# Performance work log

Measured on AMD Instinct MI355X. Metric: run time of the kernel, lower is better.

## Reference

```python
import jax, jax.numpy as jnp
import numpy as np

LATENT = 2000
N_GROUPS = 10000  # loci_count // window_size
KERNEL = 20       # window_size * 2; per-group input length is 1 so out length == KERNEL
BATCH = 128
EPS = 1e-5
SLOPE = 0.1


def setup_inputs() -> dict:
    key = jax.random.key(0)
    k1, k2, k3, k4, k5 = jax.random.split(key, 5)
    return {
        "z": jax.random.normal(k1, (BATCH, LATENT), dtype=jnp.float32),
        "W_fc": jax.random.normal(k2, (N_GROUPS, LATENT), dtype=jnp.float32) * 0.02,
        "b_fc": jax.random.normal(k3, (N_GROUPS,), dtype=jnp.float32) * 0.02,
        "gamma": jnp.ones((N_GROUPS,), dtype=jnp.float32),
        "beta": jnp.zeros((N_GROUPS,), dtype=jnp.float32),
        "conv_w": jax.random.normal(k4, (N_GROUPS, KERNEL), dtype=jnp.float32) * 0.1,
        "conv_b": jax.random.normal(k5, (N_GROUPS,), dtype=jnp.float32) * 0.02,
    }


def reference(z, W_fc, b_fc, gamma, beta, conv_w, conv_b):
    # Linear: (B, L) @ (L, G) -> (B, G)
    h = jnp.einsum("bl,gl->bg", z, W_fc) + b_fc
    # BatchNorm1d (training mode: biased batch statistics, eps=1e-5)
    mean = jnp.mean(h, axis=0)
    var = jnp.mean(jnp.square(h - mean), axis=0)
    h = (h - mean) * jax.lax.rsqrt(var + EPS) * gamma + beta
    h = jnp.where(h >= 0, h, SLOPE * h)  # LeakyReLU(0.1)
    # Grouped ConvTranspose1d with per-group input length 1 degenerates to
    # an outer product per channel: y[b,g,k] = h[b,g]*w[g,k] + b[g]
    y = h[:, :, None] * conv_w[None, :, :] + conv_b[None, :, None]  # (B, G, K)
    y = jnp.where(y >= 0, y, SLOPE * y)  # LeakyReLU(0.1)
    out = jax.nn.sigmoid(y.reshape(z.shape[0], N_GROUPS * KERNEL))
    return out
```

## Files before the change

### kernel.cpp

```cpp
#include <hip/hip_runtime.h>
#include <hip/hip_bf16.h>
#include <stdint.h>

#define BATCH 128
#define LAT   2000
#define NG    10000
#define KW    20
#define OUTW  (NG * KW)
#define EPSV  1e-5f

#define BK    64
#define NKT   32

#define EG        16
#define HR_STRIDE 132

typedef __bf16 bf16x8 __attribute__((ext_vector_type(8)));
typedef float  f32x4  __attribute__((ext_vector_type(4)));

__device__ __forceinline__ ushort f2bf(float f) {
  uint32_t u = __builtin_bit_cast(uint32_t, f);
  u = (u + 0x7FFFu + ((u >> 16) & 1u)) >> 16;
  return (ushort)u;
}

__device__ __forceinline__ int4 pack8(const float* p) {
  float4 f0 = *(const float4*)p;
  float4 f1 = *(const float4*)(p + 4);
  int4 v;
  v.x = (int)((uint32_t)f2bf(f0.x) | ((uint32_t)f2bf(f0.y) << 16));
  v.y = (int)((uint32_t)f2bf(f0.z) | ((uint32_t)f2bf(f0.w) << 16));
  v.z = (int)((uint32_t)f2bf(f1.x) | ((uint32_t)f2bf(f1.y) << 16));
  v.w = (int)((uint32_t)f2bf(f1.z) | ((uint32_t)f2bf(f1.w) << 16));
  return v;
}

__device__ __forceinline__ void gload_lds16(const void* g, void* l) {
  __builtin_amdgcn_global_load_lds(
      (const __attribute__((address_space(1))) unsigned int*)g,
      (__attribute__((address_space(3))) unsigned int*)l, 16, 0, 0);
}

__global__ __launch_bounds__(256) void zprep_kernel(
    const float* __restrict__ zp, int4* __restrict__ zswz) {
  const int cg = blockIdx.x * 256 + threadIdx.x;
  const int kt = cg >> 10;
  const int c  = cg & 1023;
  const int r  = c >> 3, j = c & 7;
  const int sc = j ^ (r & 7);
  const int k0 = kt * 64 + sc * 8;
  int4 v = make_int4(0, 0, 0, 0);
  if (k0 < LAT) v = pack8(zp + (size_t)r * LAT + k0);
  zswz[cg] = v;
}

__global__ __launch_bounds__(256, 4) void fused16_kernel(
    const int4* __restrict__ zswz, const float* __restrict__ wp,
    const float* __restrict__ gammap, const float* __restrict__ betap,
    const float* __restrict__ convwp, const float* __restrict__ convbp,
    float* __restrict__ out) {
  const int tid = threadIdx.x;
  const int g0  = blockIdx.x * EG;

  __shared__ __attribute__((aligned(16))) ushort Zs[BATCH * BK];
  __shared__ __attribute__((aligned(16))) ushort Ws[EG * BK];
  __shared__ float  h_raw[EG * HR_STRIDE];
  __shared__ float4 cw_s[EG * 5];
  __shared__ float  cb_s[EG];
  __shared__ float  scale_s[EG];
  __shared__ float  shift_s[EG];

  if (tid < EG * 5)
    cw_s[tid] = *(const float4*)(convwp + (size_t)g0 * KW + tid * 4);
  if (tid < EG) cb_s[tid] = convbp[g0 + tid];

  const int lane = tid & 63;
  const int w    = tid >> 6;
  const int q    = lane >> 4;
  const int cl   = lane & 15;

  f32x4 acc[2];
  const f32x4 vzero = {0.f, 0.f, 0.f, 0.f};
  acc[0] = vzero; acc[1] = vzero;

  for (int it = 0; it < NKT; ++it) {
    __syncthreads();

    const int4* zt = zswz + (size_t)it * 1024;
#pragma unroll
    for (int i = 0; i < 4; ++i) {
      int c = i * 256 + tid;
      gload_lds16(zt + c, &Zs[c * 8]);
    }
    if (tid < 128) {
      int r = tid >> 3, j = tid & 7;
      int gk = it * BK + j * 8;
      int4 v = make_int4(0, 0, 0, 0);
      if (gk < LAT) v = pack8(wp + (size_t)(g0 + r) * LAT + gk);
      *(int4*)&Ws[r * BK + ((j ^ (r & 7)) << 3)] = v;
    }
    __syncthreads();

#pragma unroll
    for (int kk = 0; kk < 2; ++kk) {
      int sc = kk * 4 + q;
      bf16x8 af = *(const bf16x8*)&Ws[cl * BK + ((sc ^ (cl & 7)) << 3)];
#pragma unroll
      for (int nt = 0; nt < 2; ++nt) {
        int rb = w * 32 + nt * 16 + cl;
        bf16x8 bfr = *(const bf16x8*)&Zs[rb * BK + ((sc ^ (rb & 7)) << 3)];
        acc[nt] = __builtin_amdgcn_mfma_f32_16x16x32_bf16(af, bfr, acc[nt],
                                                          0, 0, 0);
      }
    }
  }

#pragma unroll
  for (int nt = 0; nt < 2; ++nt)
#pragma unroll
    for (int r = 0; r < 4; ++r)
      h_raw[(q * 4 + r) * HR_STRIDE + w * 32 + nt * 16 + cl] = acc[nt][r];
  __syncthreads();

  float sm[2], sq[2];
#pragma unroll
  for (int half = 0; half < 2; ++half) {
    const int idx = tid + half * 256;
    const int gl  = idx >> 5;
    const int bb  = (idx & 31) * 4;
    const float4 a = *(const float4*)&h_raw[gl * HR_STRIDE + bb];
    sm[half] = a.x + a.y + a.z + a.w;
    sq[half] = a.x * a.x + a.y * a.y + a.z * a.z + a.w * a.w;
  }
#pragma unroll
  for (int m = 1; m < 32; m <<= 1) {
    sm[0] += __shfl_xor(sm[0], m); sq[0] += __shfl_xor(sq[0], m);
    sm[1] += __shfl_xor(sm[1], m); sq[1] += __shfl_xor(sq[1], m);
  }
  if ((tid & 31) == 0) {
#pragma unroll
    for (int half = 0; half < 2; ++half) {
      const int gl = (tid >> 5) + half * 8;
      float mean = sm[half] * (1.f / 128.f);
      float var  = sq[half] * (1.f / 128.f) - mean * mean;
      var = (var < 0.f) ? 0.f : var;
      float inv   = __builtin_amdgcn_rsqf(var + EPSV);
      float scale = inv * gammap[g0 + gl];
      scale_s[gl] = scale;
      shift_s[gl] = betap[g0 + gl] - mean * scale;
    }
  }
  __syncthreads();

  if (tid < 240) {
    const int col4 = tid % 80;
    const int r0   = tid / 80;
    const int gl   = col4 / 5;
    const float4 w4  = cw_s[col4];
    const float  cb  = cb_s[gl];
    const float  scl = scale_s[gl];
    const float  sft = shift_s[gl];
    const float* hsrc = &h_raw[gl * HR_STRIDE];
    float* obase = out + (size_t)g0 * KW + (size_t)col4 * 4;
    for (int j = 0; j < 43; ++j) {
      const int row = j * 3 + r0;
      if (row < BATCH) {
        float h = hsrc[row];
        h = fmaf(h, scl, sft);
        h = fmaxf(h, h * 0.1f);
        float y0 = fmaf(h, w4.x, cb);
        float y1 = fmaf(h, w4.y, cb);
        float y2 = fmaf(h, w4.z, cb);
        float y3 = fmaf(h, w4.w, cb);
        y0 = fmaxf(y0, y0 * 0.1f);
        y1 = fmaxf(y1, y1 * 0.1f);
        y2 = fmaxf(y2, y2 * 0.1f);
        y3 = fmaxf(y3, y3 * 0.1f);
        float4 ov;
        ov.x = __builtin_amdgcn_rcpf(1.f + exp2f(y0 * -1.44269504f));
        ov.y = __builtin_amdgcn_rcpf(1.f + exp2f(y1 * -1.44269504f));
        ov.z = __builtin_amdgcn_rcpf(1.f + exp2f(y2 * -1.44269504f));
        ov.w = __builtin_amdgcn_rcpf(1.f + exp2f(y3 * -1.44269504f));
        *(float4*)(obase + (size_t)row * OUTW) = ov;
      }
    }
  }
}

__global__ __launch_bounds__(256, 2) void fused_decoder_kernel(
    const float* __restrict__ zp, const float* __restrict__ wp,
    const float* __restrict__ gammap, const float* __restrict__ betap,
    const float* __restrict__ convwp, const float* __restrict__ convbp,
    float* __restrict__ out) {
  const int tid = threadIdx.x;
  const int g0  = blockIdx.x * 32;

  __shared__ ushort As[BATCH * BK];
  __shared__ ushort Bs[32 * BK];
  __shared__ float statS[2][2][16];
  __shared__ float statQ[2][2][16];

  const int lane = tid & 63;
  const int w    = tid >> 6;
  const int wm   = w & 1;
  const int wn   = w >> 1;
  const int q    = lane >> 4;
  const int cl   = lane & 15;

  f32x4 acc[4];
  const f32x4 vzero = {0.f, 0.f, 0.f, 0.f};
#pragma unroll
  for (int i = 0; i < 4; ++i) acc[i] = vzero;

  for (int it = 0; it < 32; ++it) {
    const int k0 = it * BK;
    __syncthreads();
#pragma unroll
    for (int i = 0; i < 4; ++i) {
      int c = i * 256 + tid;
      int r = c >> 3, sc = c & 7;
      int gk = k0 + sc * 8;
      int4 v = make_int4(0, 0, 0, 0);
      if (gk < LAT) v = pack8(zp + (size_t)r * LAT + gk);
      *(int4*)&As[r * BK + ((sc ^ (r & 7)) << 3)] = v;
    }
    {
      int r = tid >> 3, sc = tid & 7;
      int g  = g0 + r;
      int gk = k0 + sc * 8;
      int4 v = make_int4(0, 0, 0, 0);
      if (gk < LAT && g < NG) v = pack8(wp + (size_t)g * LAT + gk);
      *(int4*)&Bs[r * BK + ((sc ^ (r & 7)) << 3)] = v;
    }
    __syncthreads();
#pragma unroll
    for (int kk = 0; kk < 2; ++kk) {
      int sc = kk * 4 + q;
      bf16x8 af[4], bfr;
#pragma unroll
      for (int mt = 0; mt < 4; ++mt) {
        int ra = wm * 64 + mt * 16 + cl;
        af[mt] = *(const bf16x8*)&As[ra * BK + ((sc ^ (ra & 7)) << 3)];
      }
      {
        int rb = wn * 16 + cl;
        bfr = *(const bf16x8*)&Bs[rb * BK + ((sc ^ (rb & 7)) << 3)];
      }
#pragma unroll
      for (int mt = 0; mt < 4; ++mt)
        acc[mt] = __builtin_amdgcn_mfma_f32_16x16x32_bf16(af[mt], bfr,
                                                          acc[mt], 0, 0, 0);
    }
  }

  float s = 0.f, ss = 0.f;
#pragma unroll
  for (int mt = 0; mt < 4; ++mt)
#pragma unroll
    for (int r = 0; r < 4; ++r) {
      float v = acc[mt][r];
      s += v; ss += v * v;
    }
  s += __shfl_xor(s, 16); ss += __shfl_xor(ss, 16);
  s += __shfl_xor(s, 32); ss += __shfl_xor(ss, 32);
  if (q == 0) { statS[wm][wn][cl] = s; statQ[wm][wn][cl] = ss; }
  __syncthreads();

  const int gcol = g0 + wn * 16 + cl;
  const int gc   = (gcol < NG) ? gcol : (NG - 1);
  float S = statS[0][wn][cl] + statS[1][wn][cl];
  float Q = statQ[0][wn][cl] + statQ[1][wn][cl];
  float mean = S * (1.f / 128.f);
  float var  = Q * (1.f / 128.f) - mean * mean;
  var = (var < 0.f) ? 0.f : var;
  float inv = __builtin_amdgcn_rsqf(var + EPSV);
  float ga = gammap[gc], be = betap[gc], cb = convbp[gc];
  float wv[KW];
  {
    const float4* pw = (const float4*)(convwp + (size_t)gc * KW);
#pragma unroll
    for (int j = 0; j < 5; ++j) {
      float4 f = pw[j];
      wv[4 * j] = f.x; wv[4 * j + 1] = f.y;
      wv[4 * j + 2] = f.z; wv[4 * j + 3] = f.w;
    }
  }
  float scale = inv * ga;
  float shift = be - mean * scale;
  const bool ok = (gcol < NG);
#pragma unroll
  for (int mt = 0; mt < 4; ++mt) {
#pragma unroll
    for (int r = 0; r < 4; ++r) {
      float h = acc[mt][r] * scale + shift;
      h = fmaxf(h, h * 0.1f);
      int b = wm * 64 + mt * 16 + q * 4 + r;
      float4 ov[5];
#pragma unroll
      for (int j = 0; j < 5; ++j) {
        float y0 = h * wv[4 * j]     + cb;
        float y1 = h * wv[4 * j + 1] + cb;
        float y2 = h * wv[4 * j + 2] + cb;
        float y3 = h * wv[4 * j + 3] + cb;
        y0 = fmaxf(y0, y0 * 0.1f);
        y1 = fmaxf(y1, y1 * 0.1f);
        y2 = fmaxf(y2, y2 * 0.1f);
        y3 = fmaxf(y3, y3 * 0.1f);
        ov[j].x = __builtin_amdgcn_rcpf(1.f + exp2f(y0 * -1.44269504f));
        ov[j].y = __builtin_amdgcn_rcpf(1.f + exp2f(y1 * -1.44269504f));
        ov[j].z = __builtin_amdgcn_rcpf(1.f + exp2f(y2 * -1.44269504f));
        ov[j].w = __builtin_amdgcn_rcpf(1.f + exp2f(y3 * -1.44269504f));
      }
      if (ok) {
        float4* po = (float4*)(out + (size_t)b * OUTW + (size_t)gcol * KW);
#pragma unroll
        for (int j = 0; j < 5; ++j) po[j] = ov[j];
      }
    }
  }
}

extern "C" void kernel_launch(void* const* d_in, const int* in_sizes, int n_in,
                              void* d_out, int out_size, void* d_ws, size_t ws_size,
                              hipStream_t stream) {
  const float* z     = (const float*)d_in[0];
  const float* W     = (const float*)d_in[1];
  const float* gamma = (const float*)d_in[3];
  const float* beta  = (const float*)d_in[4];
  const float* convw = (const float*)d_in[5];
  const float* convb = (const float*)d_in[6];
  float* out = (float*)d_out;

  const size_t zswz_bytes = (size_t)NKT * 1024 * 16;

  if (ws_size >= zswz_bytes) {
    int4* zswz = (int4*)d_ws;
    zprep_kernel<<<128, 256, 0, stream>>>(z, zswz);
    fused16_kernel<<<NG / EG, 256, 0, stream>>>(zswz, W, gamma, beta,
                                                convw, convb, out);
  } else {
    fused_decoder_kernel<<<(NG + 31) / 32, 256, 0, stream>>>(
        z, W, gamma, beta, convw, convb, out);
  }
}
```

Measured before the change: 196.1 us.

## Replace LDS-staged GEMM loop with register-direct loads and software prefetch

The main kernel no longer stages z and W tiles through shared memory with two barriers per K step. Each lane now loads its W fragment from global memory straight into registers and converts it to bf16 in-register, with a two-step prefetch. The z fragment comes from a new row-linear bf16 buffer with a one-step prefetch. The block grows to 512 threads (8 waves, 16 batch rows each), removing LDS traffic and per-iteration synchronization, at the cost of redundant global W reads across waves (relying on cache) and more registers.

After: 258.4 us. +31.8%, slower.

```diff
diff --git a/kernel.cpp b/kernel.cpp
--- a/kernel.cpp
+++ b/kernel.cpp
@@ -9,10 +9,8 @@
 #define OUTW  (NG * KW)
 #define EPSV  1e-5f
 
-#define BK    64
 #define NKT   32
-
-#define EG        16
+#define EG    16
 #define HR_STRIDE 132
 
 typedef __bf16 bf16x8 __attribute__((ext_vector_type(8)));
@@ -35,35 +33,31 @@
   return v;
 }
 
-__device__ __forceinline__ void gload_lds16(const void* g, void* l) {
-  __builtin_amdgcn_global_load_lds(
-      (const __attribute__((address_space(1))) unsigned int*)g,
-      (__attribute__((address_space(3))) unsigned int*)l, 16, 0, 0);
+__device__ __forceinline__ bf16x8 cvt8(float4 a, float4 b) {
+  bf16x8 r;
+  r[0] = (__bf16)a.x; r[1] = (__bf16)a.y; r[2] = (__bf16)a.z; r[3] = (__bf16)a.w;
+  r[4] = (__bf16)b.x; r[5] = (__bf16)b.y; r[6] = (__bf16)b.z; r[7] = (__bf16)b.w;
+  return r;
 }
 
 __global__ __launch_bounds__(256) void zprep_kernel(
-    const float* __restrict__ zp, int4* __restrict__ zswz) {
+    const float* __restrict__ zp, int4* __restrict__ zlin) {
   const int cg = blockIdx.x * 256 + threadIdx.x;
-  const int kt = cg >> 10;
-  const int c  = cg & 1023;
-  const int r  = c >> 3, j = c & 7;
-  const int sc = j ^ (r & 7);
-  const int k0 = kt * 64 + sc * 8;
+  const int r  = cg >> 8;
+  const int k0 = (cg & 255) * 8;
   int4 v = make_int4(0, 0, 0, 0);
   if (k0 < LAT) v = pack8(zp + (size_t)r * LAT + k0);
-  zswz[cg] = v;
-}
-
-__global__ __launch_bounds__(256, 4) void fused16_kernel(
-    const int4* __restrict__ zswz, const float* __restrict__ wp,
+  zlin[cg] = v;
+}
+
+__global__ __launch_bounds__(512, 4) void fused16_kernel(
+    const int4* __restrict__ zlin, const float* __restrict__ wp,
     const float* __restrict__ gammap, const float* __restrict__ betap,
     const float* __restrict__ convwp, const float* __restrict__ convbp,
     float* __restrict__ out) {
   const int tid = threadIdx.x;
   const int g0  = blockIdx.x * EG;
 
-  __shared__ __attribute__((aligned(16))) ushort Zs[BATCH * BK];
-  __shared__ __attribute__((aligned(16))) ushort Ws[EG * BK];
   __shared__ float  h_raw[EG * HR_STRIDE];
   __shared__ float4 cw_s[EG * 5];
   __shared__ float  cb_s[EG];
@@ -78,71 +72,71 @@
   const int w    = tid >> 6;
   const int q    = lane >> 4;
   const int cl   = lane & 15;
-
-  f32x4 acc[2];
-  const f32x4 vzero = {0.f, 0.f, 0.f, 0.f};
-  acc[0] = vzero; acc[1] = vzero;
-
+  const int rb   = w * 16 + cl;
+
+  const float* wrow = wp + (size_t)(g0 + cl) * LAT;
+  const int4*  zrow = zlin + (size_t)rb * 256;
+
+  f32x4 acc = {0.f, 0.f, 0.f, 0.f};
+
+  const int koq = q * 8;
+  float4 a0 = *(const float4*)(wrow + koq);
+  float4 a1 = *(const float4*)(wrow + koq + 4);
+  float4 a2 = *(const float4*)(wrow + 32 + koq);
+  float4 a3 = *(const float4*)(wrow + 32 + koq + 4);
+  float4 b0 = *(const float4*)(wrow + 64 + koq);
+  float4 b1 = *(const float4*)(wrow + 64 + koq + 4);
+  float4 b2 = *(const float4*)(wrow + 96 + koq);
+  float4 b3 = *(const float4*)(wrow + 96 + koq + 4);
+  int4 zb0 = zrow[q];
+  int4 zb1 = zrow[4 + q];
+
+#pragma unroll 2
   for (int it = 0; it < NKT; ++it) {
-    __syncthreads();
-
-    const int4* zt = zswz + (size_t)it * 1024;
-#pragma unroll
-    for (int i = 0; i < 4; ++i) {
-      int c = i * 256 + tid;
-      gload_lds16(zt + c, &Zs[c * 8]);
-    }
-    if (tid < 128) {
-      int r = tid >> 3, j = tid & 7;
-      int gk = it * BK + j * 8;
-      int4 v = make_int4(0, 0, 0, 0);
-      if (gk < LAT) v = pack8(wp + (size_t)(g0 + r) * LAT + gk);
-      *(int4*)&Ws[r * BK + ((j ^ (r & 7)) << 3)] = v;
-    }
-    __syncthreads();
-
-#pragma unroll
-    for (int kk = 0; kk < 2; ++kk) {
-      int sc = kk * 4 + q;
-      bf16x8 af = *(const bf16x8*)&Ws[cl * BK + ((sc ^ (cl & 7)) << 3)];
-#pragma unroll
-      for (int nt = 0; nt < 2; ++nt) {
-        int rb = w * 32 + nt * 16 + cl;
-        bf16x8 bfr = *(const bf16x8*)&Zs[rb * BK + ((sc ^ (rb & 7)) << 3)];
-        acc[nt] = __builtin_amdgcn_mfma_f32_16x16x32_bf16(af, bfr, acc[nt],
-                                                          0, 0, 0);
-      }
-    }
-  }
-
-#pragma unroll
-  for (int nt = 0; nt < 2; ++nt)
-#pragma unroll
-    for (int r = 0; r < 4; ++r)
-      h_raw[(q * 4 + r) * HR_STRIDE + w * 32 + nt * 16 + cl] = acc[nt][r];
+    const int tc = (it + 2 < NKT) ? (it + 2) : (NKT - 1);
+    int kc0 = tc * 64 + koq;
+    int kc1 = tc * 64 + 32 + koq;
+    kc0 = (kc0 > LAT - 8) ? (LAT - 8) : kc0;
+    kc1 = (kc1 > LAT - 8) ? (LAT - 8) : kc1;
+    float4 c0 = *(const float4*)(wrow + kc0);
+    float4 c1 = *(const float4*)(wrow + kc0 + 4);
+    float4 c2 = *(const float4*)(wrow + kc1);
+    float4 c3 = *(const float4*)(wrow + kc1 + 4);
+    const int tn = (it + 1 < NKT) ? (it + 1) : (NKT - 1);
+    int4 zn0 = zrow[tn * 8 + q];
+    int4 zn1 = zrow[tn * 8 + 4 + q];
+
+    bf16x8 af0 = cvt8(a0, a1);
+    bf16x8 af1 = cvt8(a2, a3);
+    acc = __builtin_amdgcn_mfma_f32_16x16x32_bf16(
+        af0, __builtin_bit_cast(bf16x8, zb0), acc, 0, 0, 0);
+    acc = __builtin_amdgcn_mfma_f32_16x16x32_bf16(
+        af1, __builtin_bit_cast(bf16x8, zb1), acc, 0, 0, 0);
+
+    a0 = b0; a1 = b1; a2 = b2; a3 = b3;
+    b0 = c0; b1 = c1; b2 = c2; b3 = c3;
+    zb0 = zn0; zb1 = zn1;
+  }
+
+#pragma unroll
+  for (int r = 0; r < 4; ++r)
+    h_raw[(q * 4 + r) * HR_STRIDE + rb] = acc[r];
   __syncthreads();
 
-  float sm[2], sq[2];
-#pragma unroll
-  for (int half = 0; half < 2; ++half) {
-    const int idx = tid + half * 256;
-    const int gl  = idx >> 5;
-    const int bb  = (idx & 31) * 4;
+  {
+    const int gl = tid >> 5;
+    const int bb = (tid & 31) * 4;
     const float4 a = *(const float4*)&h_raw[gl * HR_STRIDE + bb];
-    sm[half] = a.x + a.y + a.z + a.w;
-    sq[half] = a.x * a.x + a.y * a.y + a.z * a.z + a.w * a.w;
-  }
-#pragma unroll
-  for (int m = 1; m < 32; m <<= 1) {
-    sm[0] += __shfl_xor(sm[0], m); sq[0] += __shfl_xor(sq[0], m);
-    sm[1] += __shfl_xor(sm[1], m); sq[1] += __shfl_xor(sq[1], m);
-  }
-  if ((tid & 31) == 0) {
-#pragma unroll
-    for (int half = 0; half < 2; ++half) {
-      const int gl = (tid >> 5) + half * 8;
-      float mean = sm[half] * (1.f / 128.f);
-      float var  = sq[half] * (1.f / 128.f) - mean * mean;
+    float sm = a.x + a.y + a.z + a.w;
+    float sq = a.x * a.x + a.y * a.y + a.z * a.z + a.w * a.w;
+#pragma unroll
+    for (int m = 1; m < 32; m <<= 1) {
+      sm += __shfl_xor(sm, m);
+      sq += __shfl_xor(sq, m);
+    }
+    if ((tid & 31) == 0) {
+      float mean = sm * (1.f / 128.f);
+      float var  = sq * (1.f / 128.f) - mean * mean;
       var = (var < 0.f) ? 0.f : var;
       float inv   = __builtin_amdgcn_rsqf(var + EPSV);
       float scale = inv * gammap[g0 + gl];
@@ -152,7 +146,7 @@
   }
   __syncthreads();
 
-  if (tid < 240) {
+  if (tid < 480) {
     const int col4 = tid % 80;
     const int r0   = tid / 80;
     const int gl   = col4 / 5;
@@ -162,8 +156,8 @@
     const float  sft = shift_s[gl];
     const float* hsrc = &h_raw[gl * HR_STRIDE];
     float* obase = out + (size_t)g0 * KW + (size_t)col4 * 4;
-    for (int j = 0; j < 43; ++j) {
-      const int row = j * 3 + r0;
+    for (int j = 0; j < 22; ++j) {
+      const int row = j * 6 + r0;
       if (row < BATCH) {
         float h = hsrc[row];
         h = fmaf(h, scl, sft);
@@ -187,6 +181,7 @@
   }
 }
 
+#define BKF 64
 __global__ __launch_bounds__(256, 2) void fused_decoder_kernel(
     const float* __restrict__ zp, const float* __restrict__ wp,
     const float* __restrict__ gammap, const float* __restrict__ betap,
@@ -195,8 +190,8 @@
   const int tid = threadIdx.x;
   const int g0  = blockIdx.x * 32;
 
-  __shared__ ushort As[BATCH * BK];
-  __shared__ ushort Bs[32 * BK];
+  __shared__ ushort As[BATCH * BKF];
+  __shared__ ushort Bs[32 * BKF];
   __shared__ float statS[2][2][16];
   __shared__ float statQ[2][2][16];
 
@@ -213,7 +208,7 @@
   for (int i = 0; i < 4; ++i) acc[i] = vzero;
 
   for (int it = 0; it < 32; ++it) {
-    const int k0 = it * BK;
+    const int k0 = it * BKF;
     __syncthreads();
 #pragma unroll
     for (int i = 0; i < 4; ++i) {
@@ -222,7 +217,7 @@
       int gk = k0 + sc * 8;
       int4 v = make_int4(0, 0, 0, 0);
       if (gk < LAT) v = pack8(zp + (size_t)r * LAT + gk);
-      *(int4*)&As[r * BK + ((sc ^ (r & 7)) << 3)] = v;
+      *(int4*)&As[r * BKF + ((sc ^ (r & 7)) << 3)] = v;
     }
     {
       int r = tid >> 3, sc = tid & 7;
@@ -230,7 +225,7 @@
       int gk = k0 + sc * 8;
       int4 v = make_int4(0, 0, 0, 0);
       if (gk < LAT && g < NG) v = pack8(wp + (size_t)g * LAT + gk);
-      *(int4*)&Bs[r * BK + ((sc ^ (r & 7)) << 3)] = v;
+      *(int4*)&Bs[r * BKF + ((sc ^ (r & 7)) << 3)] = v;
     }
     __syncthreads();
 #pragma unroll
@@ -240,11 +235,11 @@
 #pragma unroll
       for (int mt = 0; mt < 4; ++mt) {
         int ra = wm * 64 + mt * 16 + cl;
-        af[mt] = *(const bf16x8*)&As[ra * BK + ((sc ^ (ra & 7)) << 3)];
+        af[mt] = *(const bf16x8*)&As[ra * BKF + ((sc ^ (ra & 7)) << 3)];
       }
       {
-        int rb = wn * 16 + cl;
-        bfr = *(const bf16x8*)&Bs[rb * BK + ((sc ^ (rb & 7)) << 3)];
+        int rbx = wn * 16 + cl;
+        bfr = *(const bf16x8*)&Bs[rbx * BKF + ((sc ^ (rbx & 7)) << 3)];
       }
 #pragma unroll
       for (int mt = 0; mt < 4; ++mt)
@@ -331,12 +326,12 @@
   const float* convb = (const float*)d_in[6];
   float* out = (float*)d_out;
 
-  const size_t zswz_bytes = (size_t)NKT * 1024 * 16;
-
-  if (ws_size >= zswz_bytes) {
-    int4* zswz = (int4*)d_ws;
-    zprep_kernel<<<128, 256, 0, stream>>>(z, zswz);
-    fused16_kernel<<<NG / EG, 256, 0, stream>>>(zswz, W, gamma, beta,
+  const size_t zlin_bytes = (size_t)BATCH * 256 * 16;
+
+  if (ws_size >= zlin_bytes) {
+    int4* zlin = (int4*)d_ws;
+    zprep_kernel<<<128, 256, 0, stream>>>(z, zlin);
+    fused16_kernel<<<NG / EG, 512, 0, stream>>>(zlin, W, gamma, beta,
                                                 convw, convb, out);
   } else {
     fused_decoder_kernel<<<(NG + 31) / 32, 256, 0, stream>>>(
```
